# Kernel tuning notes

Hardware: AMD Instinct MI355X
Metric: run time of the kernel (lower is better)

## Reference

```python
import jax, jax.numpy as jnp
import numpy as np

N = 50000        # nodes
E = 1600000      # edges (avg degree 32)
F = 256          # feature_dim
H = 128          # hidden_dim
ED = 32          # edge_dim
C = 2            # num_classes
GAMMA, ZETA = -0.1, 1.1   # hard-concrete stretch bounds


def setup_inputs() -> dict:
    key = jax.random.key(0)
    ks = jax.random.split(key, 16)
    def p(i, shape, fan):
        return jax.random.normal(ks[i], shape, dtype=jnp.float32) * np.float32(1.0 / np.sqrt(fan))
    return {
        "x": jax.random.normal(ks[0], (N, F), dtype=jnp.float32),
        "edge_index": jax.random.randint(ks[1], (2, E), 0, N, dtype=jnp.int64),
        # edge scorer: Linear(2F -> ED) split into src/dst halves, then Linear(ED -> 1)
        "we_src": p(2, (F, ED), 2 * F),
        "we_dst": p(3, (F, ED), 2 * F),
        "be": jnp.zeros((ED,), jnp.float32),
        "we2": p(4, (ED,), ED),
        "be2": jnp.zeros((), jnp.float32),
        # node transform conv: Linear(F -> H)
        "wc": p(5, (F, H), F),
        "bc": jnp.zeros((H,), jnp.float32),
        # classifier: Linear(H -> H//2), LayerNorm(H//2), spectral_norm(Linear(H//2 -> C))
        "w1": p(6, (H, H // 2), H),
        "b1": jnp.zeros((H // 2,), jnp.float32),
        "ln_g": jnp.ones((H // 2,), jnp.float32),
        "ln_b": jnp.zeros((H // 2,), jnp.float32),
        "w2": p(7, (H // 2, C), H // 2),
        "b2": jnp.zeros((C,), jnp.float32),
    }


def reference(x, edge_index, we_src, we_dst, be, we2, be2, wc, bc,
              w1, b1, ln_g, ln_b, w2, b2):
    src, dst = edge_index[0], edge_index[1]
    n = x.shape[0]

    # --- edge scoring: MLP on (x_src, x_dst); project per-node first, then gather ---
    ps = x @ we_src                       # [N, ED]
    pd = x @ we_dst                       # [N, ED]
    e_h = jax.nn.relu(ps[src] + pd[dst] + be)   # [E, ED]
    logit = e_h @ we2 + be2               # [E]

    # --- hard-concrete L0 gate (deterministic / eval form) ---
    s = jax.nn.sigmoid(logit)
    gate = jnp.clip(s * (ZETA - GAMMA) + GAMMA, 0.0, 1.0)   # [E]

    # --- node transform + edge-gated message passing ---
    h = jax.nn.relu(x @ wc + bc)                            # [N, H]
    agg = jax.ops.segment_sum(gate[:, None] * h[src], dst, num_segments=n)  # [N, H]
    deg = jax.ops.segment_sum(gate, dst, num_segments=n)                    # [N]
    h_out = h + agg / (deg[:, None] + 1e-6)

    # --- edge-weighted attention pooling: attend by gated degree ---
    att = jax.nn.softmax(deg)             # [N]
    g = att @ h_out                       # [H]

    # --- classifier: Linear -> ReLU -> LayerNorm -> spectral_norm(Linear) ---
    z = jax.nn.relu(g @ w1 + b1)          # [H//2]
    mn = z.mean()
    v = ((z - mn) ** 2).mean()
    zn = (z - mn) / jnp.sqrt(v + 1e-5) * ln_g + ln_b
    sigma = jnp.linalg.norm(w2, ord=2)    # spectral norm of weight
    logits = zn @ (w2 / sigma) + b2       # [C]
    return logits
```

## Files before the change

### kernel.cpp

```cpp
#include <hip/hip_runtime.h>
#include <hip/hip_bf16.h>
#include <math.h>

constexpr int F  = 256;
constexpr int ED = 32;
constexpr int H  = 128;
constexpr int NB = 64;
constexpr int SLICE_MAX = 6272;
constexpr int CAP = 26624;
constexpr float CSH = 60.0f;

typedef __attribute__((ext_vector_type(8))) short    short8v;
typedef __attribute__((ext_vector_type(4))) float    float4v;
typedef __attribute__((ext_vector_type(8))) _Float16 half8v;

static __device__ __forceinline__ unsigned short f2bf(float f) {
    unsigned int u = __float_as_uint(f);
    unsigned int r = (u + 0x7FFFu + ((u >> 16) & 1u)) >> 16;
    return (unsigned short)r;
}

__global__ __launch_bounds__(256) void pack_kernel(
    const float* __restrict__ we_src, const float* __restrict__ we_dst,
    const float* __restrict__ wc, unsigned short* __restrict__ Wp,
    float* __restrict__ zbase, int zcount)
{
    if (blockIdx.x >= 24) {
        int zi = (blockIdx.x - 24) * 256 + threadIdx.x;
        if (zi < zcount) zbase[zi] = 0.0f;
        return;
    }
    int id = blockIdx.x * 256 + threadIdx.x;
    if (id >= 12 * 8 * 64) return;
    int lane = id & 63;
    int ks   = (id >> 6) & 7;
    int tile = id >> 9;
    int col  = tile * 16 + (lane & 15);
    int kb   = ks * 32 + (lane >> 4) * 8;

    short8v v;
    #pragma unroll
    for (int j = 0; j < 8; ++j) {
        int k = kb + j;
        float w;
        if (col < 32)       w = we_src[k * ED + col];
        else if (col < 64)  w = we_dst[k * ED + (col - 32)];
        else                w = wc[k * H + (col - 64)];
        v[j] = (short)f2bf(w);
    }
    *(short8v*)(Wp + (size_t)id * 8) = v;
}

__global__ __launch_bounds__(1024) void scatter_kernel(
    const int* __restrict__ ei, int* __restrict__ cursor,
    unsigned* __restrict__ sd, int E, int SL)
{
    __shared__ int lh[NB];
    __shared__ int lbase[NB];
    const int t = threadIdx.x;
    if (t < NB) lh[t] = 0;
    __syncthreads();

    const int e0 = blockIdx.x * 2048 + t;
    unsigned c0 = 0, c1 = 0;
    int k0 = 0, r0 = 0, k1 = 0, r1 = 0;
    const bool v0 = (e0 < E);
    const bool v1 = (e0 + 1024 < E);
    if (v0) {
        int s = ei[e0], d = ei[E + e0];
        int i = (int)((unsigned)s / (unsigned)SL);
        int j = (int)((unsigned)d / (unsigned)SL);
        k0 = i * 8 + j;
        c0 = (unsigned)(s - i * SL) | ((unsigned)(d - j * SL) << 16);
        r0 = atomicAdd(&lh[k0], 1);
    }
    if (v1) {
        int s = ei[e0 + 1024], d = ei[E + e0 + 1024];
        int i = (int)((unsigned)s / (unsigned)SL);
        int j = (int)((unsigned)d / (unsigned)SL);
        k1 = i * 8 + j;
        c1 = (unsigned)(s - i * SL) | ((unsigned)(d - j * SL) << 16);
        r1 = atomicAdd(&lh[k1], 1);
    }
    __syncthreads();
    if (t < NB && lh[t] > 0) lbase[t] = atomicAdd(&cursor[t], lh[t]);
    __syncthreads();
    if (v0) {
        int idx = lbase[k0] + r0;
        if (idx < CAP) sd[(size_t)k0 * CAP + idx] = c0;
    }
    if (v1) {
        int idx = lbase[k1] + r1;
        if (idx < CAP) sd[(size_t)k1 * CAP + idx] = c1;
    }
}

__global__ __launch_bounds__(256) void gemm_kernel(
    const float* __restrict__ x, const unsigned short* __restrict__ Wp,
    const float* __restrict__ bc,
    _Float16* __restrict__ psh, _Float16* __restrict__ pdh,
    _Float16* __restrict__ hh, int M16)
{
    __shared__ __align__(16) unsigned char As[16 * 512];

    const int t    = threadIdx.x;
    const int w    = t >> 6;
    const int lane = t & 63;

    const short8v* WpV = (const short8v*)Wp;
    short8v Bfr[3][8];
    #pragma unroll
    for (int ct = 0; ct < 3; ++ct)
        #pragma unroll
        for (int ks = 0; ks < 8; ++ks)
            Bfr[ct][ks] = WpV[(((w * 3 + ct) * 8 + ks) << 6) + lane];

    const int srow = t >> 4;
    const int sseg = t & 15;
    const int ssw  = (srow & 7) << 4;

    const int arow = lane & 15;
    const int asw  = (arow & 7) << 4;
    const int akb  = (lane >> 4) * 16;

    const int crow0 = (lane >> 4) * 4;
    const int ccol  = lane & 15;

    for (int rt = blockIdx.x; rt < M16; rt += gridDim.x) {
        const int n0 = rt * 16;
        {
            const float4* src = (const float4*)(x + (size_t)(n0 + srow) * F + sseg * 16);
            float4 f0 = src[0], f1 = src[1], f2 = src[2], f3 = src[3];
            short8v lo, hi;
            lo[0] = (short)f2bf(f0.x); lo[1] = (short)f2bf(f0.y);
            lo[2] = (short)f2bf(f0.z); lo[3] = (short)f2bf(f0.w);
            lo[4] = (short)f2bf(f1.x); lo[5] = (short)f2bf(f1.y);
            lo[6] = (short)f2bf(f1.z); lo[7] = (short)f2bf(f1.w);
            hi[0] = (short)f2bf(f2.x); hi[1] = (short)f2bf(f2.y);
            hi[2] = (short)f2bf(f2.z); hi[3] = (short)f2bf(f2.w);
            hi[4] = (short)f2bf(f3.x); hi[5] = (short)f2bf(f3.y);
            hi[6] = (short)f2bf(f3.z); hi[7] = (short)f2bf(f3.w);
            *(short8v*)&As[srow * 512 + ((sseg * 32 +  0) ^ ssw)] = lo;
            *(short8v*)&As[srow * 512 + ((sseg * 32 + 16) ^ ssw)] = hi;
        }
        __syncthreads();

        float4v accs[3];
        #pragma unroll
        for (int ct = 0; ct < 3; ++ct) accs[ct] = (float4v){0.f, 0.f, 0.f, 0.f};

        #pragma unroll
        for (int ks = 0; ks < 8; ++ks) {
            short8v a = *(const short8v*)&As[arow * 512 + ((ks * 64 + akb) ^ asw)];
            accs[0] = __builtin_amdgcn_mfma_f32_16x16x32_bf16(a, Bfr[0][ks], accs[0], 0, 0, 0);
            accs[1] = __builtin_amdgcn_mfma_f32_16x16x32_bf16(a, Bfr[1][ks], accs[1], 0, 0, 0);
            accs[2] = __builtin_amdgcn_mfma_f32_16x16x32_bf16(a, Bfr[2][ks], accs[2], 0, 0, 0);
        }

        #pragma unroll
        for (int ct = 0; ct < 3; ++ct) {
            const int gcol = w * 48 + ct * 16 + ccol;
            #pragma unroll
            for (int r = 0; r < 4; ++r) {
                const int row = n0 + crow0 + r;
                float v = accs[ct][r];
                if (gcol < 32) {
                    psh[(size_t)row * ED + gcol] = (_Float16)v;
                } else if (gcol < 64) {
                    pdh[(size_t)row * ED + (gcol - 32)] = (_Float16)v;
                } else {
                    float b = bc[gcol - 64];
                    hh[(size_t)row * H + (gcol - 64)] = (_Float16)fmaxf(v + b, 0.f);
                }
            }
        }
        __syncthreads();
    }
}

__global__ __launch_bounds__(1024) void edge_gate_kernel(
    const unsigned* __restrict__ sd, const int* __restrict__ cnt,
    const _Float16* __restrict__ psh, const _Float16* __restrict__ pdh,
    const float* __restrict__ be, const float* __restrict__ we2,
    const float* __restrict__ be2,
    float* __restrict__ gate, float* __restrict__ deg, int N, int SL)
{
    __shared__ float sbe[ED], swe2[ED];
    __shared__ float sdeg[SLICE_MAX];
    const int t = threadIdx.x;
    if (t < ED) { sbe[t] = be[t]; swe2[t] = we2[t]; }
    for (int idx = t; idx < SLICE_MAX; idx += 1024) sdeg[idx] = 0.0f;
    __syncthreads();

    const int j = blockIdx.x & 7;
    const int k = blockIdx.x >> 3;
    const int i = k >> 3;
    const int p = k & 7;
    const int bucket = i * 8 + j;
    const int start = bucket * CAP;
    const int len   = min(cnt[bucket], CAP);
    const int cs = start + (len * p) / 8;
    const int ce = start + (len * (p + 1)) / 8;
    const int ibase = i * SL;
    const int jbase = j * SL;
    const int jlen  = min(SL, N - jbase);
    const int seg = t & 3;

    for (int base = cs; base < ce; base += 256) {
        const int e = base + (t >> 2);
        if (e < ce) {
            const unsigned code = sd[e];
            const int sl = (int)(code & 0xFFFFu);
            const int dl = (int)(code >> 16);
            half8v a  = *(const half8v*)(psh + (size_t)(ibase + sl) * ED + seg * 8);
            half8v bb = *(const half8v*)(pdh + (size_t)(jbase + dl) * ED + seg * 8);
            float part = 0.f;
            #pragma unroll
            for (int jj = 0; jj < 8; ++jj) {
                int kk = seg * 8 + jj;
                part += fmaxf((float)a[jj] + (float)bb[jj] + sbe[kk], 0.f) * swe2[kk];
            }
            part += __shfl_xor(part, 1);
            part += __shfl_xor(part, 2);
            if (seg == 0) {
                float logit = part + be2[0];
                float sg = 1.0f / (1.0f + expf(-logit));
                float gt = fminf(fmaxf(sg * 1.2f - 0.1f, 0.0f), 1.0f);
                gate[e] = gt;
                if (gt > 0.0f) atomicAdd(&sdeg[dl], gt);
            }
        }
    }
    __syncthreads();

    float* dst = deg + jbase;
    for (int idx = t; idx < jlen; idx += 1024) {
        float v = sdeg[idx];
        if (v != 0.0f) atomicAdd(&dst[idx], v);
    }
}

__global__ __launch_bounds__(256) void stats_sum_kernel(
    const float* __restrict__ deg, float* __restrict__ S, int N)
{
    float sum = 0.0f;
    for (int i = blockIdx.x * 256 + threadIdx.x; i < N; i += gridDim.x * 256)
        sum += expf(deg[i] - CSH);
    #pragma unroll
    for (int k = 1; k < 64; k <<= 1) sum += __shfl_xor(sum, k);
    if ((threadIdx.x & 63) == 0) atomicAdd(S, sum);
}

__global__ __launch_bounds__(1024) void edge_u_kernel(
    const unsigned* __restrict__ sd, const int* __restrict__ cnt,
    const float* __restrict__ gate, const float* __restrict__ deg,
    const float* __restrict__ S,
    float* __restrict__ u, int N, int SL)
{
    __shared__ float su[SLICE_MAX];
    const int t = threadIdx.x;
    for (int idx = t; idx < SLICE_MAX; idx += 1024) su[idx] = 0.0f;
    __syncthreads();

    const float invS = 1.0f / S[0];

    const int j = blockIdx.x & 7;
    const int k = blockIdx.x >> 3;
    const int i = k >> 3;
    const int p = k & 7;
    const int bucket = i * 8 + j;
    const int start = bucket * CAP;
    const int len   = min(cnt[bucket], CAP);
    const int cs = start + (len * p) / 8;
    const int ce = start + (len * (p + 1)) / 8;
    const int ibase = i * SL;
    const int jbase = j * SL;
    const int ilen  = min(SL, N - ibase);

    for (int e = cs + t; e < ce; e += 1024) {
        float gt = gate[e];
        if (gt != 0.f) {
            unsigned code = sd[e];
            int sl = (int)(code & 0xFFFFu);
            int dl = (int)(code >> 16);
            float dg = deg[jbase + dl];
            float cv = expf(dg - CSH) * invS / (dg + 1e-6f);
            atomicAdd(&su[sl], gt * cv);
        }
    }
    __syncthreads();

    float* dst = u + ibase;
    for (int idx = t; idx < ilen; idx += 1024) {
        float v = su[idx];
        if (v != 0.0f) atomicAdd(&dst[idx], v);
    }
}

__global__ __launch_bounds__(256) void pool_kernel(
    const _Float16* __restrict__ hh, const float* __restrict__ deg,
    const float* __restrict__ S, const float* __restrict__ u,
    float* __restrict__ gacc, int N)
{
    __shared__ float red[16][128];
    const int t = threadIdx.x;
    const int lane = t & 15;
    const int row  = t >> 4;

    const float invS = 1.0f / S[0];

    float acc[8];
    #pragma unroll
    for (int q = 0; q < 8; ++q) acc[q] = 0.f;

    for (int n = blockIdx.x * 16 + row; n < N; n += gridDim.x * 16) {
        float wgt = expf(deg[n] - CSH) * invS + u[n];
        half8v hv = *(const half8v*)(hh + (size_t)n * H + lane * 8);
        #pragma unroll
        for (int q = 0; q < 8; ++q) acc[q] += wgt * (float)hv[q];
    }
    #pragma unroll
    for (int q = 0; q < 8; ++q) red[row][lane * 8 + q] = acc[q];
    __syncthreads();
    if (t < 128) {
        float s = 0.f;
        #pragma unroll
        for (int r = 0; r < 16; ++r) s += red[r][t];
        atomicAdd(&gacc[t], s);
    }
}

__global__ __launch_bounds__(64) void cls_kernel(
    const float* __restrict__ gacc, const float* __restrict__ w1,
    const float* __restrict__ b1, const float* __restrict__ ln_g,
    const float* __restrict__ ln_b, const float* __restrict__ w2,
    const float* __restrict__ b2, float* __restrict__ out)
{
    __shared__ float gs[H];
    const int t = threadIdx.x;
    gs[t] = gacc[t];
    gs[t + 64] = gacc[t + 64];
    __syncthreads();

    float acc = b1[t];
    #pragma unroll 4
    for (int k = 0; k < H; ++k) acc += gs[k] * w1[k * 64 + t];
    float z = fmaxf(acc, 0.f);

    float sm = z;
    #pragma unroll
    for (int m = 1; m < 64; m <<= 1) sm += __shfl_xor(sm, m);
    float mn = sm * (1.0f / 64.0f);
    float dv = (z - mn) * (z - mn);
    float sv = dv;
    #pragma unroll
    for (int m = 1; m < 64; m <<= 1) sv += __shfl_xor(sv, m);
    float var = sv * (1.0f / 64.0f);

    float zn = (z - mn) * rsqrtf(var + 1e-5f) * ln_g[t] + ln_b[t];

    float w20 = w2[t * 2 + 0];
    float w21 = w2[t * 2 + 1];
    float ga = w20 * w20, gb = w20 * w21, gc = w21 * w21;
    float p0 = zn * w20, p1 = zn * w21;
    #pragma unroll
    for (int m = 1; m < 64; m <<= 1) {
        ga += __shfl_xor(ga, m);
        gb += __shfl_xor(gb, m);
        gc += __shfl_xor(gc, m);
        p0 += __shfl_xor(p0, m);
        p1 += __shfl_xor(p1, m);
    }
    if (t == 0) {
        float tr = ga + gc;
        float df = ga - gc;
        float eig = 0.5f * (tr + sqrtf(df * df + 4.0f * gb * gb));
        float sigma = sqrtf(eig);
        out[0] = p0 / sigma + b2[0];
        out[1] = p1 / sigma + b2[1];
    }
}

extern "C" void kernel_launch(void* const* d_in, const int* in_sizes, int n_in,
                              void* d_out, int out_size, void* d_ws, size_t ws_size,
                              hipStream_t stream) {
    const float* x      = (const float*)d_in[0];
    const int*   ei     = (const int*)  d_in[1];
    const float* we_src = (const float*)d_in[2];
    const float* we_dst = (const float*)d_in[3];
    const float* be     = (const float*)d_in[4];
    const float* we2    = (const float*)d_in[5];
    const float* be2    = (const float*)d_in[6];
    const float* wc     = (const float*)d_in[7];
    const float* bc     = (const float*)d_in[8];
    const float* w1     = (const float*)d_in[9];
    const float* b1     = (const float*)d_in[10];
    const float* ln_g   = (const float*)d_in[11];
    const float* ln_b   = (const float*)d_in[12];
    const float* w2     = (const float*)d_in[13];
    const float* b2     = (const float*)d_in[14];

    const int N = in_sizes[0] / F;
    const int E = in_sizes[1] / 2;
    const int M16 = N / 16;
    const int SL = (N + 7) / 8;

    float* ws = (float*)d_ws;
    size_t off = 0;
    float* zbase = ws;
    float* deg  = ws + off; off += (size_t)N;
    float* u    = ws + off; off += (size_t)N;
    float* gacc = ws + off; off += 128;
    float* S    = ws + off; off += 1;
    int*   cursor = (int*)(ws + off); off += NB;
    const int zcount = (int)off;
    off = (off + 15) & ~(size_t)15;
    unsigned short* Wp = (unsigned short*)(ws + off); off += (12 * 8 * 64 * 8) / 2;
    off = (off + 15) & ~(size_t)15;
    _Float16* psh = (_Float16*)(ws + off); off += (size_t)N * ED / 2;
    _Float16* pdh = (_Float16*)(ws + off); off += (size_t)N * ED / 2;
    _Float16* hh  = (_Float16*)(ws + off); off += (size_t)N * H / 2;
    float* gate = ws + off; off += (size_t)NB * CAP;
    unsigned* sd = (unsigned*)(ws + off); off += (size_t)NB * CAP;

    const int zblocks = (zcount + 255) / 256;
    pack_kernel<<<24 + zblocks, 256, 0, stream>>>(we_src, we_dst, wc, Wp, zbase, zcount);
    scatter_kernel<<<(E + 2047) / 2048, 1024, 0, stream>>>(ei, cursor, sd, E, SL);
    gemm_kernel<<<1024, 256, 0, stream>>>(x, Wp, bc, psh, pdh, hh, M16);
    edge_gate_kernel<<<512, 1024, 0, stream>>>(sd, cursor, psh, pdh, be, we2, be2,
                                               gate, deg, N, SL);
    stats_sum_kernel<<<256, 256, 0, stream>>>(deg, S, N);
    edge_u_kernel<<<512, 1024, 0, stream>>>(sd, cursor, gate, deg, S, u, N, SL);
    pool_kernel<<<256, 256, 0, stream>>>(hh, deg, S, u, gacc, N);
    cls_kernel<<<1, 64, 0, stream>>>(gacc, w1, b1, ln_g, ln_b, w2, b2, (float*)d_out);
}
```

Before: 142.6 us.

## Fuse edge gating, softmax stats, u-scatter, pooling and classifier into cooperative kernel

```diff
diff --git a/kernel.cpp b/kernel.cpp
--- a/kernel.cpp
+++ b/kernel.cpp
@@ -1,6 +1,9 @@
 #include <hip/hip_runtime.h>
 #include <hip/hip_bf16.h>
+#include <hip/hip_cooperative_groups.h>
 #include <math.h>
+
+namespace cg = cooperative_groups;
 
 constexpr int F  = 256;
 constexpr int ED = 32;
@@ -8,6 +11,7 @@
 constexpr int NB = 64;
 constexpr int SLICE_MAX = 6272;
 constexpr int CAP = 26624;
+constexpr int GL_MAX = 6720;
 constexpr float CSH = 60.0f;
 
 typedef __attribute__((ext_vector_type(8))) short    short8v;
@@ -178,34 +182,47 @@
     }
 }
 
-__global__ __launch_bounds__(1024) void edge_gate_kernel(
+__global__ __launch_bounds__(1024) void mega_kernel(
     const unsigned* __restrict__ sd, const int* __restrict__ cnt,
     const _Float16* __restrict__ psh, const _Float16* __restrict__ pdh,
     const float* __restrict__ be, const float* __restrict__ we2,
     const float* __restrict__ be2,
-    float* __restrict__ gate, float* __restrict__ deg, int N, int SL)
+    float* __restrict__ deg, float* __restrict__ S, float* __restrict__ u,
+    const _Float16* __restrict__ hh, float* __restrict__ gacc,
+    const float* __restrict__ w1, const float* __restrict__ b1,
+    const float* __restrict__ ln_g, const float* __restrict__ ln_b,
+    const float* __restrict__ w2, const float* __restrict__ b2,
+    float* __restrict__ out, int N, int SL)
 {
     __shared__ float sbe[ED], swe2[ED];
     __shared__ float sdeg[SLICE_MAX];
-    const int t = threadIdx.x;
+    __shared__ _Float16 gate_lds[GL_MAX];
+    __shared__ float red[128];
+
+    cg::grid_group grid = cg::this_grid();
+
+    const int t   = threadIdx.x;
+    const int bid = blockIdx.x;
+
+    const int j = bid & 7;
+    const int k = bid >> 3;
+    const int i = k >> 2;
+    const int p = k & 3;
+    const int bucket = i * 8 + j;
+    const int start = bucket * CAP;
+    const int len   = min(cnt[bucket], CAP);
+    const int cs = start + (len * p) / 4;
+    const int ce = start + (len * (p + 1)) / 4;
+    const int ibase = i * SL;
+    const int jbase = j * SL;
+    const int jlen  = min(SL, N - jbase);
+    const int ilen  = min(SL, N - ibase);
+
     if (t < ED) { sbe[t] = be[t]; swe2[t] = we2[t]; }
     for (int idx = t; idx < SLICE_MAX; idx += 1024) sdeg[idx] = 0.0f;
     __syncthreads();
 
-    const int j = blockIdx.x & 7;
-    const int k = blockIdx.x >> 3;
-    const int i = k >> 3;
-    const int p = k & 7;
-    const int bucket = i * 8 + j;
-    const int start = bucket * CAP;
-    const int len   = min(cnt[bucket], CAP);
-    const int cs = start + (len * p) / 8;
-    const int ce = start + (len * (p + 1)) / 8;
-    const int ibase = i * SL;
-    const int jbase = j * SL;
-    const int jlen  = min(SL, N - jbase);
     const int seg = t & 3;
-
     for (int base = cs; base < ce; base += 256) {
         const int e = base + (t >> 2);
         if (e < ce) {
@@ -226,158 +243,132 @@
                 float logit = part + be2[0];
                 float sg = 1.0f / (1.0f + expf(-logit));
                 float gt = fminf(fmaxf(sg * 1.2f - 0.1f, 0.0f), 1.0f);
-                gate[e] = gt;
+                gate_lds[e - cs] = (_Float16)gt;
                 if (gt > 0.0f) atomicAdd(&sdeg[dl], gt);
             }
         }
     }
     __syncthreads();
-
-    float* dst = deg + jbase;
-    for (int idx = t; idx < jlen; idx += 1024) {
-        float v = sdeg[idx];
-        if (v != 0.0f) atomicAdd(&dst[idx], v);
-    }
-}
-
-__global__ __launch_bounds__(256) void stats_sum_kernel(
-    const float* __restrict__ deg, float* __restrict__ S, int N)
-{
-    float sum = 0.0f;
-    for (int i = blockIdx.x * 256 + threadIdx.x; i < N; i += gridDim.x * 256)
-        sum += expf(deg[i] - CSH);
-    #pragma unroll
-    for (int k = 1; k < 64; k <<= 1) sum += __shfl_xor(sum, k);
-    if ((threadIdx.x & 63) == 0) atomicAdd(S, sum);
-}
-
-__global__ __launch_bounds__(1024) void edge_u_kernel(
-    const unsigned* __restrict__ sd, const int* __restrict__ cnt,
-    const float* __restrict__ gate, const float* __restrict__ deg,
-    const float* __restrict__ S,
-    float* __restrict__ u, int N, int SL)
-{
-    __shared__ float su[SLICE_MAX];
-    const int t = threadIdx.x;
-    for (int idx = t; idx < SLICE_MAX; idx += 1024) su[idx] = 0.0f;
-    __syncthreads();
-
-    const float invS = 1.0f / S[0];
-
-    const int j = blockIdx.x & 7;
-    const int k = blockIdx.x >> 3;
-    const int i = k >> 3;
-    const int p = k & 7;
-    const int bucket = i * 8 + j;
-    const int start = bucket * CAP;
-    const int len   = min(cnt[bucket], CAP);
-    const int cs = start + (len * p) / 8;
-    const int ce = start + (len * (p + 1)) / 8;
-    const int ibase = i * SL;
-    const int jbase = j * SL;
-    const int ilen  = min(SL, N - ibase);
-
-    for (int e = cs + t; e < ce; e += 1024) {
-        float gt = gate[e];
-        if (gt != 0.f) {
-            unsigned code = sd[e];
-            int sl = (int)(code & 0xFFFFu);
-            int dl = (int)(code >> 16);
-            float dg = deg[jbase + dl];
-            float cv = expf(dg - CSH) * invS / (dg + 1e-6f);
-            atomicAdd(&su[sl], gt * cv);
-        }
-    }
-    __syncthreads();
-
-    float* dst = u + ibase;
-    for (int idx = t; idx < ilen; idx += 1024) {
-        float v = su[idx];
-        if (v != 0.0f) atomicAdd(&dst[idx], v);
-    }
-}
-
-__global__ __launch_bounds__(256) void pool_kernel(
-    const _Float16* __restrict__ hh, const float* __restrict__ deg,
-    const float* __restrict__ S, const float* __restrict__ u,
-    float* __restrict__ gacc, int N)
-{
-    __shared__ float red[16][128];
-    const int t = threadIdx.x;
-    const int lane = t & 15;
-    const int row  = t >> 4;
-
-    const float invS = 1.0f / S[0];
-
-    float acc[8];
-    #pragma unroll
-    for (int q = 0; q < 8; ++q) acc[q] = 0.f;
-
-    for (int n = blockIdx.x * 16 + row; n < N; n += gridDim.x * 16) {
-        float wgt = expf(deg[n] - CSH) * invS + u[n];
-        half8v hv = *(const half8v*)(hh + (size_t)n * H + lane * 8);
-        #pragma unroll
-        for (int q = 0; q < 8; ++q) acc[q] += wgt * (float)hv[q];
-    }
-    #pragma unroll
-    for (int q = 0; q < 8; ++q) red[row][lane * 8 + q] = acc[q];
-    __syncthreads();
-    if (t < 128) {
-        float s = 0.f;
-        #pragma unroll
-        for (int r = 0; r < 16; ++r) s += red[r][t];
-        atomicAdd(&gacc[t], s);
-    }
-}
-
-__global__ __launch_bounds__(64) void cls_kernel(
-    const float* __restrict__ gacc, const float* __restrict__ w1,
-    const float* __restrict__ b1, const float* __restrict__ ln_g,
-    const float* __restrict__ ln_b, const float* __restrict__ w2,
-    const float* __restrict__ b2, float* __restrict__ out)
-{
-    __shared__ float gs[H];
-    const int t = threadIdx.x;
-    gs[t] = gacc[t];
-    gs[t + 64] = gacc[t + 64];
-    __syncthreads();
-
-    float acc = b1[t];
-    #pragma unroll 4
-    for (int k = 0; k < H; ++k) acc += gs[k] * w1[k * 64 + t];
-    float z = fmaxf(acc, 0.f);
-
-    float sm = z;
-    #pragma unroll
-    for (int m = 1; m < 64; m <<= 1) sm += __shfl_xor(sm, m);
-    float mn = sm * (1.0f / 64.0f);
-    float dv = (z - mn) * (z - mn);
-    float sv = dv;
-    #pragma unroll
-    for (int m = 1; m < 64; m <<= 1) sv += __shfl_xor(sv, m);
-    float var = sv * (1.0f / 64.0f);
-
-    float zn = (z - mn) * rsqrtf(var + 1e-5f) * ln_g[t] + ln_b[t];
-
-    float w20 = w2[t * 2 + 0];
-    float w21 = w2[t * 2 + 1];
-    float ga = w20 * w20, gb = w20 * w21, gc = w21 * w21;
-    float p0 = zn * w20, p1 = zn * w21;
-    #pragma unroll
-    for (int m = 1; m < 64; m <<= 1) {
-        ga += __shfl_xor(ga, m);
-        gb += __shfl_xor(gb, m);
-        gc += __shfl_xor(gc, m);
-        p0 += __shfl_xor(p0, m);
-        p1 += __shfl_xor(p1, m);
-    }
-    if (t == 0) {
-        float tr = ga + gc;
-        float df = ga - gc;
-        float eig = 0.5f * (tr + sqrtf(df * df + 4.0f * gb * gb));
-        float sigma = sqrtf(eig);
-        out[0] = p0 / sigma + b2[0];
-        out[1] = p1 / sigma + b2[1];
+    for (int idx = t; idx < SLICE_MAX; idx += 1024) {
+        if (idx < jlen) {
+            float v = sdeg[idx];
+            if (v != 0.0f) atomicAdd(&deg[jbase + idx], v);
+        }
+        sdeg[idx] = 0.0f;
+    }
+
+    grid.sync();
+
+    {
+        float sum = 0.0f;
+        int idx = bid * 1024 + t;
+        if (idx < N) sum = expf(deg[idx] - CSH);
+        #pragma unroll
+        for (int m = 1; m < 64; m <<= 1) sum += __shfl_xor(sum, m);
+        if ((t & 63) == 0 && sum != 0.0f) atomicAdd(S, sum);
+    }
+
+    grid.sync();
+
+    {
+        const float invS = 1.0f / S[0];
+        for (int e = cs + t; e < ce; e += 1024) {
+            float gt = (float)gate_lds[e - cs];
+            if (gt != 0.f) {
+                unsigned code = sd[e];
+                int sl = (int)(code & 0xFFFFu);
+                int dl = (int)(code >> 16);
+                float dg = deg[jbase + dl];
+                float cv = expf(dg - CSH) * invS / (dg + 1e-6f);
+                atomicAdd(&sdeg[sl], gt * cv);
+            }
+        }
+        __syncthreads();
+        for (int idx = t; idx < ilen; idx += 1024) {
+            float v = sdeg[idx];
+            if (v != 0.0f) atomicAdd(&u[ibase + idx], v);
+        }
+    }
+
+    grid.sync();
+
+    {
+        const float invS = 1.0f / S[0];
+        const int lane16 = t & 15;
+        const int row    = t >> 4;
+        float acc[8];
+        #pragma unroll
+        for (int q = 0; q < 8; ++q) acc[q] = 0.f;
+
+        for (int n = bid * 64 + row; n < N; n += 256 * 64) {
+            float wgt = expf(deg[n] - CSH) * invS + u[n];
+            half8v hv = *(const half8v*)(hh + (size_t)n * H + lane16 * 8);
+            #pragma unroll
+            for (int q = 0; q < 8; ++q) acc[q] += wgt * (float)hv[q];
+        }
+        #pragma unroll
+        for (int q = 0; q < 8; ++q) {
+            acc[q] += __shfl_xor(acc[q], 16);
+            acc[q] += __shfl_xor(acc[q], 32);
+        }
+        if (t < 128) red[t] = 0.0f;
+        __syncthreads();
+        if ((t & 63) < 16) {
+            #pragma unroll
+            for (int q = 0; q < 8; ++q)
+                atomicAdd(&red[lane16 * 8 + q], acc[q]);
+        }
+        __syncthreads();
+        if (t < 128) {
+            float v = red[t];
+            if (v != 0.0f) atomicAdd(&gacc[t], v);
+        }
+    }
+
+    grid.sync();
+
+    if (bid == 0) {
+        if (t < 128) red[t] = gacc[t];
+        __syncthreads();
+        if (t < 64) {
+            float acc = b1[t];
+            #pragma unroll 4
+            for (int kk = 0; kk < H; ++kk) acc += red[kk] * w1[kk * 64 + t];
+            float z = fmaxf(acc, 0.f);
+
+            float sm = z;
+            #pragma unroll
+            for (int m = 1; m < 64; m <<= 1) sm += __shfl_xor(sm, m);
+            float mn = sm * (1.0f / 64.0f);
+            float dv = (z - mn) * (z - mn);
+            float sv = dv;
+            #pragma unroll
+            for (int m = 1; m < 64; m <<= 1) sv += __shfl_xor(sv, m);
+            float var = sv * (1.0f / 64.0f);
+
+            float zn = (z - mn) * rsqrtf(var + 1e-5f) * ln_g[t] + ln_b[t];
+
+            float w20 = w2[t * 2 + 0];
+            float w21 = w2[t * 2 + 1];
+            float ga = w20 * w20, gb = w20 * w21, gc = w21 * w21;
+            float p0 = zn * w20, p1 = zn * w21;
+            #pragma unroll
+            for (int m = 1; m < 64; m <<= 1) {
+                ga += __shfl_xor(ga, m);
+                gb += __shfl_xor(gb, m);
+                gc += __shfl_xor(gc, m);
+                p0 += __shfl_xor(p0, m);
+                p1 += __shfl_xor(p1, m);
+            }
+            if (t == 0) {
+                float tr = ga + gc;
+                float df = ga - gc;
+                float eig = 0.5f * (tr + sqrtf(df * df + 4.0f * gb * gb));
+                float sigma = sqrtf(eig);
+                out[0] = p0 / sigma + b2[0];
+                out[1] = p1 / sigma + b2[1];
+            }
+        }
     }
 }
 
@@ -420,17 +411,23 @@
     _Float16* psh = (_Float16*)(ws + off); off += (size_t)N * ED / 2;
     _Float16* pdh = (_Float16*)(ws + off); off += (size_t)N * ED / 2;
     _Float16* hh  = (_Float16*)(ws + off); off += (size_t)N * H / 2;
-    float* gate = ws + off; off += (size_t)NB * CAP;
     unsigned* sd = (unsigned*)(ws + off); off += (size_t)NB * CAP;
+    float* outp = (float*)d_out;
 
     const int zblocks = (zcount + 255) / 256;
     pack_kernel<<<24 + zblocks, 256, 0, stream>>>(we_src, we_dst, wc, Wp, zbase, zcount);
     scatter_kernel<<<(E + 2047) / 2048, 1024, 0, stream>>>(ei, cursor, sd, E, SL);
     gemm_kernel<<<1024, 256, 0, stream>>>(x, Wp, bc, psh, pdh, hh, M16);
-    edge_gate_kernel<<<512, 1024, 0, stream>>>(sd, cursor, psh, pdh, be, we2, be2,
-                                               gate, deg, N, SL);
-    stats_sum_kernel<<<256, 256, 0, stream>>>(deg, S, N);
-    edge_u_kernel<<<512, 1024, 0, stream>>>(sd, cursor, gate, deg, S, u, N, SL);
-    pool_kernel<<<256, 256, 0, stream>>>(hh, deg, S, u, gacc, N);
-    cls_kernel<<<1, 64, 0, stream>>>(gacc, w1, b1, ln_g, ln_b, w2, b2, (float*)d_out);
-}
+
+    int Nv = N, SLv = SL;
+    void* args[] = {
+        (void*)&sd, (void*)&cursor, (void*)&psh, (void*)&pdh,
+        (void*)&be, (void*)&we2, (void*)&be2,
+        (void*)&deg, (void*)&S, (void*)&u,
+        (void*)&hh, (void*)&gacc,
+        (void*)&w1, (void*)&b1, (void*)&ln_g, (void*)&ln_b,
+        (void*)&w2, (void*)&b2, (void*)&outp, (void*)&Nv, (void*)&SLv
+    };
+    hipLaunchCooperativeKernel((void*)mega_kernel, dim3(256), dim3(1024),
+                               args, 0, stream);
+}
```

After: 220.8 us. 1.55x slower.

## Defer softmax normalization, fuse stats and classifier into pool, store gates as fp16

Applied to the files above, without the earlier changes.

```diff
diff --git a/kernel.cpp b/kernel.cpp
--- a/kernel.cpp
+++ b/kernel.cpp
@@ -183,7 +183,7 @@
     const _Float16* __restrict__ psh, const _Float16* __restrict__ pdh,
     const float* __restrict__ be, const float* __restrict__ we2,
     const float* __restrict__ be2,
-    float* __restrict__ gate, float* __restrict__ deg, int N, int SL)
+    _Float16* __restrict__ gateh, float* __restrict__ deg, int N, int SL)
 {
     __shared__ float sbe[ED], swe2[ED];
     __shared__ float sdeg[SLICE_MAX];
@@ -226,7 +226,7 @@
                 float logit = part + be2[0];
                 float sg = 1.0f / (1.0f + expf(-logit));
                 float gt = fminf(fmaxf(sg * 1.2f - 0.1f, 0.0f), 1.0f);
-                gate[e] = gt;
+                gateh[e] = (_Float16)gt;
                 if (gt > 0.0f) atomicAdd(&sdeg[dl], gt);
             }
         }
@@ -240,29 +240,15 @@
     }
 }
 
-__global__ __launch_bounds__(256) void stats_sum_kernel(
-    const float* __restrict__ deg, float* __restrict__ S, int N)
-{
-    float sum = 0.0f;
-    for (int i = blockIdx.x * 256 + threadIdx.x; i < N; i += gridDim.x * 256)
-        sum += expf(deg[i] - CSH);
-    #pragma unroll
-    for (int k = 1; k < 64; k <<= 1) sum += __shfl_xor(sum, k);
-    if ((threadIdx.x & 63) == 0) atomicAdd(S, sum);
-}
-
 __global__ __launch_bounds__(1024) void edge_u_kernel(
     const unsigned* __restrict__ sd, const int* __restrict__ cnt,
-    const float* __restrict__ gate, const float* __restrict__ deg,
-    const float* __restrict__ S,
-    float* __restrict__ u, int N, int SL)
+    const _Float16* __restrict__ gateh, const float* __restrict__ deg,
+    float* __restrict__ uraw, int N, int SL)
 {
     __shared__ float su[SLICE_MAX];
     const int t = threadIdx.x;
     for (int idx = t; idx < SLICE_MAX; idx += 1024) su[idx] = 0.0f;
     __syncthreads();
-
-    const float invS = 1.0f / S[0];
 
     const int j = blockIdx.x & 7;
     const int k = blockIdx.x >> 3;
@@ -278,47 +264,57 @@
     const int ilen  = min(SL, N - ibase);
 
     for (int e = cs + t; e < ce; e += 1024) {
-        float gt = gate[e];
+        float gt = (float)gateh[e];
         if (gt != 0.f) {
             unsigned code = sd[e];
             int sl = (int)(code & 0xFFFFu);
             int dl = (int)(code >> 16);
             float dg = deg[jbase + dl];
-            float cv = expf(dg - CSH) * invS / (dg + 1e-6f);
+            float cv = expf(dg - CSH) / (dg + 1e-6f);
             atomicAdd(&su[sl], gt * cv);
         }
     }
     __syncthreads();
 
-    float* dst = u + ibase;
+    float* dst = uraw + ibase;
     for (int idx = t; idx < ilen; idx += 1024) {
         float v = su[idx];
         if (v != 0.0f) atomicAdd(&dst[idx], v);
     }
 }
 
-__global__ __launch_bounds__(256) void pool_kernel(
+__global__ __launch_bounds__(256) void pool_cls_kernel(
     const _Float16* __restrict__ hh, const float* __restrict__ deg,
-    const float* __restrict__ S, const float* __restrict__ u,
-    float* __restrict__ gacc, int N)
+    const float* __restrict__ uraw,
+    float* __restrict__ gacc, float* __restrict__ S, int* __restrict__ done,
+    const float* __restrict__ w1, const float* __restrict__ b1,
+    const float* __restrict__ ln_g, const float* __restrict__ ln_b,
+    const float* __restrict__ w2, const float* __restrict__ b2,
+    float* __restrict__ out, int N)
 {
     __shared__ float red[16][128];
+    __shared__ bool lastf;
     const int t = threadIdx.x;
     const int lane = t & 15;
     const int row  = t >> 4;
 
-    const float invS = 1.0f / S[0];
-
     float acc[8];
     #pragma unroll
     for (int q = 0; q < 8; ++q) acc[q] = 0.f;
+    float sexp = 0.f;
 
     for (int n = blockIdx.x * 16 + row; n < N; n += gridDim.x * 16) {
-        float wgt = expf(deg[n] - CSH) * invS + u[n];
+        float ex  = expf(deg[n] - CSH);
+        float wgt = ex + uraw[n];
         half8v hv = *(const half8v*)(hh + (size_t)n * H + lane * 8);
         #pragma unroll
         for (int q = 0; q < 8; ++q) acc[q] += wgt * (float)hv[q];
-    }
+        if (lane == 0) sexp += ex;
+    }
+    sexp += __shfl_xor(sexp, 16);
+    sexp += __shfl_xor(sexp, 32);
+    if ((t & 63) == 0 && sexp != 0.f) atomicAdd(S, sexp);
+
     #pragma unroll
     for (int q = 0; q < 8; ++q) red[row][lane * 8 + q] = acc[q];
     __syncthreads();
@@ -326,58 +322,60 @@
         float s = 0.f;
         #pragma unroll
         for (int r = 0; r < 16; ++r) s += red[r][t];
-        atomicAdd(&gacc[t], s);
-    }
-}
-
-__global__ __launch_bounds__(64) void cls_kernel(
-    const float* __restrict__ gacc, const float* __restrict__ w1,
-    const float* __restrict__ b1, const float* __restrict__ ln_g,
-    const float* __restrict__ ln_b, const float* __restrict__ w2,
-    const float* __restrict__ b2, float* __restrict__ out)
-{
-    __shared__ float gs[H];
-    const int t = threadIdx.x;
-    gs[t] = gacc[t];
-    gs[t + 64] = gacc[t + 64];
-    __syncthreads();
-
-    float acc = b1[t];
-    #pragma unroll 4
-    for (int k = 0; k < H; ++k) acc += gs[k] * w1[k * 64 + t];
-    float z = fmaxf(acc, 0.f);
-
-    float sm = z;
-    #pragma unroll
-    for (int m = 1; m < 64; m <<= 1) sm += __shfl_xor(sm, m);
-    float mn = sm * (1.0f / 64.0f);
-    float dv = (z - mn) * (z - mn);
-    float sv = dv;
-    #pragma unroll
-    for (int m = 1; m < 64; m <<= 1) sv += __shfl_xor(sv, m);
-    float var = sv * (1.0f / 64.0f);
-
-    float zn = (z - mn) * rsqrtf(var + 1e-5f) * ln_g[t] + ln_b[t];
-
-    float w20 = w2[t * 2 + 0];
-    float w21 = w2[t * 2 + 1];
-    float ga = w20 * w20, gb = w20 * w21, gc = w21 * w21;
-    float p0 = zn * w20, p1 = zn * w21;
-    #pragma unroll
-    for (int m = 1; m < 64; m <<= 1) {
-        ga += __shfl_xor(ga, m);
-        gb += __shfl_xor(gb, m);
-        gc += __shfl_xor(gc, m);
-        p0 += __shfl_xor(p0, m);
-        p1 += __shfl_xor(p1, m);
-    }
-    if (t == 0) {
-        float tr = ga + gc;
-        float df = ga - gc;
-        float eig = 0.5f * (tr + sqrtf(df * df + 4.0f * gb * gb));
-        float sigma = sqrtf(eig);
-        out[0] = p0 / sigma + b2[0];
-        out[1] = p1 / sigma + b2[1];
+        if (s != 0.f) atomicAdd(&gacc[t], s);
+    }
+
+    __threadfence();
+    __syncthreads();
+    if (t == 0) lastf = (atomicAdd(done, 1) == (int)gridDim.x - 1);
+    __syncthreads();
+    if (!lastf) return;
+
+    const float invS = 1.0f / atomicAdd(S, 0.0f);
+    float* gs = &red[0][0];
+    if (t < 64) {
+        gs[t]      = atomicAdd(&gacc[t], 0.0f)      * invS;
+        gs[t + 64] = atomicAdd(&gacc[t + 64], 0.0f) * invS;
+    }
+    __syncthreads();
+    if (t < 64) {
+        float acc2 = b1[t];
+        #pragma unroll 4
+        for (int kk = 0; kk < H; ++kk) acc2 += gs[kk] * w1[kk * 64 + t];
+        float z = fmaxf(acc2, 0.f);
+
+        float sm = z;
+        #pragma unroll
+        for (int m = 1; m < 64; m <<= 1) sm += __shfl_xor(sm, m);
+        float mn = sm * (1.0f / 64.0f);
+        float dv = (z - mn) * (z - mn);
+        float sv = dv;
+        #pragma unroll
+        for (int m = 1; m < 64; m <<= 1) sv += __shfl_xor(sv, m);
+        float var = sv * (1.0f / 64.0f);
+
+        float zn = (z - mn) * rsqrtf(var + 1e-5f) * ln_g[t] + ln_b[t];
+
+        float w20 = w2[t * 2 + 0];
+        float w21 = w2[t * 2 + 1];
+        float ga = w20 * w20, gb = w20 * w21, gc = w21 * w21;
+        float p0 = zn * w20, p1 = zn * w21;
+        #pragma unroll
+        for (int m = 1; m < 64; m <<= 1) {
+            ga += __shfl_xor(ga, m);
+            gb += __shfl_xor(gb, m);
+            gc += __shfl_xor(gc, m);
+            p0 += __shfl_xor(p0, m);
+            p1 += __shfl_xor(p1, m);
+        }
+        if (t == 0) {
+            float tr = ga + gc;
+            float df = ga - gc;
+            float eig = 0.5f * (tr + sqrtf(df * df + 4.0f * gb * gb));
+            float sigma = sqrtf(eig);
+            out[0] = p0 / sigma + b2[0];
+            out[1] = p1 / sigma + b2[1];
+        }
     }
 }
 
@@ -409,9 +407,10 @@
     size_t off = 0;
     float* zbase = ws;
     float* deg  = ws + off; off += (size_t)N;
-    float* u    = ws + off; off += (size_t)N;
+    float* uraw = ws + off; off += (size_t)N;
     float* gacc = ws + off; off += 128;
     float* S    = ws + off; off += 1;
+    int*   done = (int*)(ws + off); off += 1;
     int*   cursor = (int*)(ws + off); off += NB;
     const int zcount = (int)off;
     off = (off + 15) & ~(size_t)15;
@@ -420,7 +419,7 @@
     _Float16* psh = (_Float16*)(ws + off); off += (size_t)N * ED / 2;
     _Float16* pdh = (_Float16*)(ws + off); off += (size_t)N * ED / 2;
     _Float16* hh  = (_Float16*)(ws + off); off += (size_t)N * H / 2;
-    float* gate = ws + off; off += (size_t)NB * CAP;
+    _Float16* gateh = (_Float16*)(ws + off); off += (size_t)NB * CAP / 2;
     unsigned* sd = (unsigned*)(ws + off); off += (size_t)NB * CAP;
 
     const int zblocks = (zcount + 255) / 256;
@@ -428,9 +427,9 @@
     scatter_kernel<<<(E + 2047) / 2048, 1024, 0, stream>>>(ei, cursor, sd, E, SL);
     gemm_kernel<<<1024, 256, 0, stream>>>(x, Wp, bc, psh, pdh, hh, M16);
     edge_gate_kernel<<<512, 1024, 0, stream>>>(sd, cursor, psh, pdh, be, we2, be2,
-                                               gate, deg, N, SL);
-    stats_sum_kernel<<<256, 256, 0, stream>>>(deg, S, N);
-    edge_u_kernel<<<512, 1024, 0, stream>>>(sd, cursor, gate, deg, S, u, N, SL);
-    pool_kernel<<<256, 256, 0, stream>>>(hh, deg, S, u, gacc, N);
-    cls_kernel<<<1, 64, 0, stream>>>(gacc, w1, b1, ln_g, ln_b, w2, b2, (float*)d_out);
-}
+                                               gateh, deg, N, SL);
+    edge_u_kernel<<<512, 1024, 0, stream>>>(sd, cursor, gateh, deg, uraw, N, SL);
+    pool_cls_kernel<<<256, 256, 0, stream>>>(hh, deg, uraw, gacc, S, done,
+                                             w1, b1, ln_g, ln_b, w2, b2,
+                                             (float*)d_out, N);
+}
```

Measured after the change: 147.6 us. +3.5%, slower.
